# Optimization experiments

Hardware: AMD Instinct MI355X
Metric: run time of the kernel (lower is better)

## Reference

```python
import jax, jax.numpy as jnp
import numpy as np

B = 4; IMG = 32; P = 2; CIN = 3; G = IMG // P; N = G * G; D = 768; NL = 8
DI = 1536; NH = 24; HD = 64; DS = 128; CONVDIM = DI + 2 * DS; DPROJ = 2 * DI + 2 * DS + NH
OUTC = 3 * CIN; FREQ = 256; EPS = 1e-6


def _sincos_1d(dim, pos):
    omega = np.arange(dim // 2, dtype=np.float64) / (dim / 2.0)
    omega = 1.0 / 10000 ** omega
    out = np.einsum('m,d->md', pos.reshape(-1), omega)
    return np.concatenate([np.sin(out), np.cos(out)], axis=1)


def _pos_embed_2d(dim, gs):
    gh = np.arange(gs, dtype=np.float32)
    gw = np.arange(gs, dtype=np.float32)
    grid = np.stack(np.meshgrid(gw, gh), axis=0)
    return np.concatenate([_sincos_1d(dim // 2, grid[0]), _sincos_1d(dim // 2, grid[1])], axis=1)


POS = jnp.asarray(_pos_embed_2d(D, G), dtype=jnp.float32)[None]  # [1, N, D]


def _ln(x):
    m = x.mean(-1, keepdims=True)
    v = ((x - m) ** 2).mean(-1, keepdims=True)
    return (x - m) * jax.lax.rsqrt(v + EPS)


def _patch_embed(img, w, b):
    # conv with kernel=stride=P == reshape to (c, ph, pw)-ordered patch vectors + matmul
    xp = img.reshape(B, CIN, G, P, G, P).transpose(0, 2, 4, 1, 3, 5).reshape(B, N, CIN * P * P)
    return xp @ w + b


def _t_embed(t, tw1, tb1, tw2, tb2):
    half = FREQ // 2
    freqs = jnp.exp(-jnp.log(10000.0) * jnp.arange(half, dtype=jnp.float32) / half)
    args = t[:, None] * freqs[None]
    emb = jnp.concatenate([jnp.cos(args), jnp.sin(args)], axis=-1)
    return jax.nn.silu(emb @ tw1 + tb1) @ tw2 + tb2


def _mamba2(u, in_w, conv_w, conv_b, dt_bias, A_log, D_ssm, out_w):
    # u: [B, N, D]
    zxbcdt = u @ in_w                           # [B, N, DPROJ]
    z = zxbcdt[..., :DI]
    xBC = zxbcdt[..., DI:DI + CONVDIM]
    dt_raw = zxbcdt[..., DI + CONVDIM:]
    # causal depthwise conv1d, kernel 4
    pad = jnp.pad(xBC, ((0, 0), (3, 0), (0, 0)))
    xBC = sum(pad[:, k:k + N, :] * conv_w[:, k] for k in range(4)) + conv_b
    xBC = jax.nn.silu(xBC)
    xs = xBC[..., :DI].reshape(B, N, NH, HD)
    Bm = xBC[..., DI:DI + DS]
    Cm = xBC[..., DI + DS:]
    dt = jax.nn.softplus(dt_raw + dt_bias)       # [B, N, NH]
    a = dt * (-jnp.exp(A_log))                   # [B, N, NH], negative
    acum = jnp.cumsum(a, axis=1)
    seg = acum[:, :, None, :] - acum[:, None, :, :]   # [B, l, s, NH]
    tril = jnp.tril(jnp.ones((N, N), bool))
    decay = jnp.exp(jnp.where(tril[None, :, :, None], seg, -1e30))
    decay = jnp.moveaxis(decay, -1, 1)           # [B, NH, l, s]
    CB = jnp.einsum('bln,bsn->bls', Cm, Bm)
    scores = CB[:, None] * decay * jnp.moveaxis(dt, -1, 1)[:, :, None, :]
    y = jnp.einsum('bhls,bshp->blhp', scores, xs) + D_ssm[None, None, :, None] * xs
    y = y.reshape(B, N, DI) * jax.nn.silu(z)
    return y @ out_w


def _conv3(x, w, b):
    o = jax.lax.conv_general_dilated(x, w, (1, 1), 'SAME',
                                     dimension_numbers=('NCHW', 'OIHW', 'NCHW'))
    return o + b[None, :, None, None]


def _hfnet(h, w1, b1, w2, b2, w3, b3):
    c = jax.nn.relu(_conv3(h, w1, b1))
    c = jax.nn.relu(_conv3(c, w2, b2))
    return h + _conv3(c, w3, b3)


def _forward(x, t, y, H1, H2, H3, xe_w, xe_b, ye_w, ye_b, tw1, tb1, tw2, tb2,
             adaln_w, adaln_b, in_w, conv_w, conv_b, dt_bias, A_log, D_ssm, out_w,
             fl_t_w, fl_t_b, fl_y_w, fl_y_b, fl_lin_w, fl_lin_b,
             e1_w1, e1_b1, e1_w2, e1_b2, e1_w3, e1_b3,
             e2_w1, e2_b1, e2_w2, e2_b2, e2_w3, e2_b3,
             e3_w1, e3_b1, e3_w2, e3_b2, e3_w3, e3_b3):
    xe = _patch_embed(x, xe_w, xe_b) + POS
    ye = _patch_embed(y, ye_w, ye_b) + POS
    te = _t_embed(t, tw1, tb1, tw2, tb2)
    st = jax.nn.silu(te)          # [B, D]
    sy = jax.nn.silu(ye)          # [B, N, D]

    def layer(xc, p):
        aw, ab, iw, cw, cb, db, al, dd, ow = p
        sh_t, sc_t, g_t = jnp.split(st @ aw + ab, 3, axis=-1)
        sh_y, sc_y, g_y = jnp.split(sy @ aw + ab, 3, axis=-1)
        shift = sh_t[:, None] + sh_y
        scale = sc_t[:, None] + sc_y
        gate = g_t[:, None] + g_y
        xm = _ln(xc) * (1.0 + scale) + shift
        return gate * _mamba2(xm, iw, cw, cb, db, al, dd, ow) + xc, None

    xh, _ = jax.lax.scan(layer, xe, (adaln_w, adaln_b, in_w, conv_w, conv_b,
                                     dt_bias, A_log, D_ssm, out_w))
    sh_t, sc_t = jnp.split(st @ fl_t_w + fl_t_b, 2, axis=-1)
    sh_y, sc_y = jnp.split(sy @ fl_y_w + fl_y_b, 2, axis=-1)
    xf = (_ln(xh) * (1.0 + sc_t[:, None] + sc_y) + sh_t[:, None] + sh_y) @ fl_lin_w + fl_lin_b
    # unpatchify: nhwpqc -> nchpwq
    img = xf.reshape(B, G, G, P, P, OUTC).transpose(0, 5, 1, 3, 2, 4).reshape(B, OUTC, IMG, IMG)
    h1 = _hfnet(H1, e1_w1, e1_b1, e1_w2, e1_b2, e1_w3, e1_b3)
    h2 = _hfnet(H2, e2_w1, e2_b1, e2_w2, e2_b2, e2_w3, e2_b3)
    h3 = _hfnet(H3, e3_w1, e3_b1, e3_w2, e3_b2, e3_w3, e3_b3)
    return (img, h1, h2, h3)


def setup_inputs() -> dict:
    ks = iter(jax.random.split(jax.random.key(0), 80))
    def nrm(shape, s=0.02):
        return jax.random.normal(next(ks), shape, jnp.float32) * s
    z = lambda *s: jnp.zeros(s, jnp.float32)
    inp = {}
    inp['x'] = jax.random.normal(next(ks), (B, CIN, IMG, IMG), jnp.float32)
    inp['t'] = jax.random.uniform(next(ks), (B,), jnp.float32) * 1000.0
    inp['y'] = jax.random.normal(next(ks), (B, CIN, IMG, IMG), jnp.float32)
    inp['H1'] = jax.random.normal(next(ks), (B, CIN, IMG, IMG), jnp.float32)
    inp['H2'] = jax.random.normal(next(ks), (B, CIN, IMG, IMG), jnp.float32)
    inp['H3'] = jax.random.normal(next(ks), (B, CIN, IMG, IMG), jnp.float32)
    inp['xe_w'] = nrm((CIN * P * P, D), 0.1); inp['xe_b'] = z(D)
    inp['ye_w'] = nrm((CIN * P * P, D), 0.1); inp['ye_b'] = z(D)
    inp['tw1'] = nrm((FREQ, D)); inp['tb1'] = z(D)
    inp['tw2'] = nrm((D, D)); inp['tb2'] = z(D)
    inp['adaln_w'] = nrm((NL, D, 3 * D)); inp['adaln_b'] = nrm((NL, 3 * D))
    inp['in_w'] = nrm((NL, D, DPROJ))
    inp['conv_w'] = nrm((NL, CONVDIM, 4), 0.2); inp['conv_b'] = z(NL, CONVDIM)
    inp['dt_bias'] = nrm((NL, NH), 0.5)
    inp['A_log'] = jnp.tile(jnp.log(jnp.arange(1.0, NH + 1.0, dtype=jnp.float32)), (NL, 1))
    inp['D_ssm'] = jnp.ones((NL, NH), jnp.float32)
    inp['out_w'] = nrm((NL, DI, D))
    inp['fl_t_w'] = nrm((D, 2 * D)); inp['fl_t_b'] = z(2 * D)
    inp['fl_y_w'] = nrm((D, 2 * D)); inp['fl_y_b'] = z(2 * D)
    inp['fl_lin_w'] = nrm((D, P * P * OUTC)); inp['fl_lin_b'] = z(P * P * OUTC)
    for i in (1, 2, 3):
        inp['e%d_w1' % i] = nrm((64, CIN, 3, 3), 0.1); inp['e%d_b1' % i] = z(64)
        inp['e%d_w2' % i] = nrm((64, 64, 3, 3), 0.05); inp['e%d_b2' % i] = z(64)
        inp['e%d_w3' % i] = nrm((CIN, 64, 3, 3), 0.05); inp['e%d_b3' % i] = z(CIN)
    return inp


def reference(x, t, y, H1, H2, H3, xe_w, xe_b, ye_w, ye_b, tw1, tb1, tw2, tb2,
              adaln_w, adaln_b, in_w, conv_w, conv_b, dt_bias, A_log, D_ssm, out_w,
              fl_t_w, fl_t_b, fl_y_w, fl_y_b, fl_lin_w, fl_lin_b,
              e1_w1, e1_b1, e1_w2, e1_b2, e1_w3, e1_b3,
              e2_w1, e2_b1, e2_w2, e2_b2, e2_w3, e2_b3,
              e3_w1, e3_b1, e3_w2, e3_b2, e3_w3, e3_b3):
    return _forward(x, t, y, H1, H2, H3, xe_w, xe_b, ye_w, ye_b, tw1, tb1, tw2, tb2,
                    adaln_w, adaln_b, in_w, conv_w, conv_b, dt_bias, A_log, D_ssm, out_w,
                    fl_t_w, fl_t_b, fl_y_w, fl_y_b, fl_lin_w, fl_lin_b,
                    e1_w1, e1_b1, e1_w2, e1_b2, e1_w3, e1_b3,
                    e2_w1, e2_b1, e2_w2, e2_b2, e2_w3, e2_b3,
                    e3_w1, e3_b1, e3_w2, e3_b2, e3_w3, e3_b3)
```

## Files before the change

### kernel.cpp

```cpp
#include <hip/hip_runtime.h>
#include <cmath>

namespace {

constexpr int kB = 4;
constexpr int kN = 256;
constexpr int kD = 768;
constexpr int kNL = 8;
constexpr int kDI = 1536;
constexpr int kNH = 24;
constexpr int kHD = 64;
constexpr int kCONV = 1792;
constexpr int kDPROJ = 3352;
constexpr int kD3 = 2304;
constexpr int kNCAT = 19968;
constexpr int kOFF_FL = 18432;

typedef __attribute__((ext_vector_type(8))) short short8;
typedef __attribute__((ext_vector_type(4))) float f32x4;

__device__ __forceinline__ float siluf(float x) { return x / (1.f + expf(-x)); }

__device__ __forceinline__ short f2bf(float f) {
  unsigned u = __float_as_uint(f);
  unsigned r = (u + 0x7fffu + ((u >> 16) & 1u)) >> 16;
  return (short)r;
}

__device__ __forceinline__ void gload_lds16(const void* g, void* l) {
  __builtin_amdgcn_global_load_lds(
      (const __attribute__((address_space(1))) void*)g,
      (__attribute__((address_space(3))) void*)l, 16, 0, 0);
}

template <int N> __device__ __forceinline__ void wait_barrier();
template <> __device__ __forceinline__ void wait_barrier<0>() {
  asm volatile("s_waitcnt vmcnt(0)\n\ts_barrier" ::: "memory");
}
template <> __device__ __forceinline__ void wait_barrier<2>() {
  asm volatile("s_waitcnt vmcnt(2)\n\ts_barrier" ::: "memory");
}
template <> __device__ __forceinline__ void wait_barrier<3>() {
  asm volatile("s_waitcnt vmcnt(3)\n\ts_barrier" ::: "memory");
}
template <> __device__ __forceinline__ void wait_barrier<4>() {
  asm volatile("s_waitcnt vmcnt(4)\n\ts_barrier" ::: "memory");
}

__global__ void patch_embed2_kernel(const float* __restrict__ img0,
                                    const float* __restrict__ w0,
                                    const float* __restrict__ b0,
                                    float* __restrict__ out0,
                                    const float* __restrict__ img1,
                                    const float* __restrict__ w1,
                                    const float* __restrict__ b1,
                                    float* __restrict__ out1,
                                    short* __restrict__ out1_bf) {
  int gid = blockIdx.x * blockDim.x + threadIdx.x;
  if (gid >= kB * kN * kD) return;
  int z = blockIdx.z;
  const float* img = z ? img1 : img0;
  const float* w = z ? w1 : w0;
  const float* bias = z ? b1 : b0;
  int d = gid % kD;
  int n = (gid / kD) % kN;
  int b = gid / (kD * kN);
  int gi = n >> 4, gj = n & 15;
  float acc = bias[d];
#pragma unroll
  for (int c = 0; c < 3; ++c)
#pragma unroll
    for (int pi = 0; pi < 2; ++pi)
#pragma unroll
      for (int pj = 0; pj < 2; ++pj) {
        float v = img[((b * 3 + c) * 32 + gi * 2 + pi) * 32 + gj * 2 + pj];
        acc += v * w[(c * 4 + pi * 2 + pj) * kD + d];
      }
  float pos;
  if (d < 192)       pos = sinf((float)gj * powf(10000.f, -(float)d / 192.f));
  else if (d < 384)  pos = cosf((float)gj * powf(10000.f, -(float)(d - 192) / 192.f));
  else if (d < 576)  pos = sinf((float)gi * powf(10000.f, -(float)(d - 384) / 192.f));
  else               pos = cosf((float)gi * powf(10000.f, -(float)(d - 576) / 192.f));
  acc += pos;
  if (z) {
    float v = siluf(acc);
    out1[gid] = v;
    out1_bf[gid] = f2bf(v);
  } else {
    out0[gid] = acc;
  }
}

__global__ void tembed_args_kernel(const float* __restrict__ t,
                                   float* __restrict__ ctst) {
  int idx = blockIdx.x * 256 + threadIdx.x;
  if (idx >= kB * 256) return;
  int b = idx >> 8, j = idx & 255;
  int k = j & 127;
  float f = expf(-9.210340371976184f * (float)k / 128.f);
  float arg = t[b] * f;
  ctst[idx] = (j < 128) ? cosf(arg) : sinf(arg);
}

__global__ __launch_bounds__(256) void splitk_mm_stage1(
    const float* __restrict__ A, const float* __restrict__ W,
    float* __restrict__ part, int K, int Nn, int KC) {
  int n = blockIdx.x * 256 + threadIdx.x;
  int kc = blockIdx.y;
  int l = blockIdx.z;
  if (n >= Nn) return;
  const float* w = W + (size_t)l * K * Nn + (size_t)kc * 64 * Nn + n;
  int kb = kc * 64;
  float a0 = 0.f, a1 = 0.f, a2 = 0.f, a3 = 0.f;
  for (int k = 0; k < 64; ++k) {
    float wv = w[(size_t)k * Nn];
    a0 += A[0 * K + kb + k] * wv;
    a1 += A[1 * K + kb + k] * wv;
    a2 += A[2 * K + kb + k] * wv;
    a3 += A[3 * K + kb + k] * wv;
  }
  size_t base = (((size_t)l * KC + kc) * 4) * Nn + n;
  part[base] = a0;
  part[base + Nn] = a1;
  part[base + 2 * (size_t)Nn] = a2;
  part[base + 3 * (size_t)Nn] = a3;
}

__global__ void splitk_mm_reduce(const float* __restrict__ part,
                                 const float* __restrict__ bias,
                                 float* __restrict__ C, int Nn, int KC, int L,
                                 int act) {
  int idx = blockIdx.x * 256 + threadIdx.x;
  if (idx >= L * 4 * Nn) return;
  int n = idx % Nn;
  int b = (idx / Nn) & 3;
  int l = idx / (4 * Nn);
  float s = bias[(size_t)l * Nn + n];
  for (int kc = 0; kc < KC; ++kc)
    s += part[(((size_t)l * KC + kc) * 4 + b) * Nn + n];
  C[idx] = act ? siluf(s) : s;
}

__global__ __launch_bounds__(256) void transposeW_kernel(
    const float* __restrict__ W, short* __restrict__ Wt, int K, int N,
    size_t sW, size_t sWt) {
  W += (size_t)blockIdx.z * sW;
  Wt += (size_t)blockIdx.z * sWt;
  __shared__ float tile[32][33];
  int n0 = blockIdx.x * 32, k0 = blockIdx.y * 32;
  int tid = threadIdx.x;
  int tx = tid & 31, ty = tid >> 5;
#pragma unroll
  for (int i = 0; i < 4; ++i) {
    int k = k0 + ty + i * 8;
    int n = n0 + tx;
    tile[ty + i * 8][tx] = (n < N) ? W[(size_t)k * N + n] : 0.f;
  }
  __syncthreads();
#pragma unroll
  for (int i = 0; i < 4; ++i) {
    int n = n0 + ty + i * 8;
    int k = k0 + tx;
    Wt[(size_t)n * K + k] = f2bf(tile[tx][ty + i * 8]);
  }
}

__global__ void concat_bias_kernel(const float* __restrict__ a,
                                   const float* __restrict__ b,
                                   float* __restrict__ dst) {
  int i = blockIdx.x * 256 + threadIdx.x;
  if (i < kOFF_FL) dst[i] = a[i];
  else if (i < kNCAT) dst[i] = b[i - kOFF_FL];
}

template <int BM, int BN>
__global__ __launch_bounds__(256) void mfma_gemm(
    const short* __restrict__ A, const short* __restrict__ Bt,
    const float* __restrict__ bias, float* __restrict__ C,
    int Nn, int Ksplit, int Ktot, int ldc, size_t czstride) {
  constexpr int MI = BM / 32;
  constexpr int NJ = BN / 32;
  constexpr int LPW = BM / 64 + BN / 64;
  __shared__ short Als[3 * BM * 32];
  __shared__ short Bls[3 * BN * 32];
  int m0 = blockIdx.y * BM, n0 = blockIdx.x * BN;
  int koff = blockIdx.z * Ksplit;
  C += (size_t)blockIdx.z * czstride;
  int tid = threadIdx.x;
  int lane = tid & 63, wid = tid >> 6;
  int wr = wid >> 1, wc = wid & 1;
  f32x4 acc[MI][NJ] = {};
  int sm = tid >> 2;
  int sk = (tid & 3) * 8;
  const int nsteps = Ksplit >> 5;
  auto stage = [&](int buf, int k0) {
#pragma unroll
    for (int h = 0; h < BM / 64; ++h)
      gload_lds16(&A[(size_t)(m0 + h * 64 + sm) * Ktot + koff + k0 + sk],
                  &Als[buf * (BM * 32) + h * 2048 + wid * 512]);
#pragma unroll
    for (int h = 0; h < BN / 64; ++h)
      gload_lds16(&Bt[(size_t)(n0 + h * 64 + sm) * Ktot + koff + k0 + sk],
                  &Bls[buf * (BN * 32) + h * 2048 + wid * 512]);
  };
  stage(0, 0);
  if (nsteps > 1) stage(1, 32);
  int cur = 0;
  for (int s = 0; s < nsteps; ++s) {
    if (s + 1 < nsteps) wait_barrier<LPW>();
    else wait_barrier<0>();
    if (s + 2 < nsteps) stage(cur == 0 ? 2 : cur - 1, (s + 2) << 5);
    short8 av[MI], bv[NJ];
#pragma unroll
    for (int mi = 0; mi < MI; ++mi)
      av[mi] = *(const short8*)&Als[cur * (BM * 32) +
                                    (wr * (BM / 2) + mi * 16 + (lane & 15)) *
                                        32 +
                                    (lane >> 4) * 8];
#pragma unroll
    for (int nj = 0; nj < NJ; ++nj)
      bv[nj] = *(const short8*)&Bls[cur * (BN * 32) +
                                    (wc * (BN / 2) + nj * 16 + (lane & 15)) *
                                        32 +
                                    (lane >> 4) * 8];
#pragma unroll
    for (int mi = 0; mi < MI; ++mi)
#pragma unroll
      for (int nj = 0; nj < NJ; ++nj)
        acc[mi][nj] = __builtin_amdgcn_mfma_f32_16x16x32_bf16(
            av[mi], bv[nj], acc[mi][nj], 0, 0, 0);
    cur = (cur == 2) ? 0 : cur + 1;
  }
#pragma unroll
  for (int mi = 0; mi < MI; ++mi)
#pragma unroll
    for (int nj = 0; nj < NJ; ++nj)
#pragma unroll
      for (int r = 0; r < 4; ++r) {
        int gm = m0 + wr * (BM / 2) + mi * 16 + (lane >> 4) * 4 + r;
        int gn = n0 + wc * (BN / 2) + nj * 16 + (lane & 15);
        if (gn >= Nn) continue;
        C[(size_t)gm * ldc + gn] = acc[mi][nj][r] + (bias ? bias[gn] : 0.f);
      }
}

__global__ __launch_bounds__(256) void cb_mfma_kernel(
    const short* __restrict__ bC, const short* __restrict__ bB,
    float* __restrict__ CBp) {
  constexpr int K = 128;
  __shared__ short Als[128 * 32];
  __shared__ short Bls[128 * 32];
  int b = blockIdx.z;
  int m0 = blockIdx.y * 128, n0 = blockIdx.x * 128;
  if (n0 >= m0 + 128) return;
  const short* A = bC + (size_t)b * 256 * K;
  const short* Bt = bB + (size_t)b * 256 * K;
  int tid = threadIdx.x;
  int lane = tid & 63, wid = tid >> 6;
  int wr = wid >> 1, wc = wid & 1;
  f32x4 acc[4][4] = {};
  int sm = tid >> 2;
  int sk = (tid & 3) * 8;
  for (int k0 = 0; k0 < K; k0 += 32) {
    __syncthreads();
    gload_lds16(&A[(size_t)(m0 + sm) * K + k0 + sk], &Als[wid * 512]);
    gload_lds16(&A[(size_t)(m0 + 64 + sm) * K + k0 + sk],
                &Als[2048 + wid * 512]);
    gload_lds16(&Bt[(size_t)(n0 + sm) * K + k0 + sk], &Bls[wid * 512]);
    gload_lds16(&Bt[(size_t)(n0 + 64 + sm) * K + k0 + sk],
                &Bls[2048 + wid * 512]);
    __syncthreads();
    short8 av[4], bv[4];
#pragma unroll
    for (int mi = 0; mi < 4; ++mi)
      av[mi] = *(const short8*)&Als[(wr * 64 + mi * 16 + (lane & 15)) * 32 +
                                    (lane >> 4) * 8];
#pragma unroll
    for (int nj = 0; nj < 4; ++nj)
      bv[nj] = *(const short8*)&Bls[(wc * 64 + nj * 16 + (lane & 15)) * 32 +
                                    (lane >> 4) * 8];
#pragma unroll
    for (int mi = 0; mi < 4; ++mi)
#pragma unroll
      for (int nj = 0; nj < 4; ++nj)
        acc[mi][nj] = __builtin_amdgcn_mfma_f32_16x16x32_bf16(
            av[mi], bv[nj], acc[mi][nj], 0, 0, 0);
  }
#pragma unroll
  for (int mi = 0; mi < 4; ++mi)
#pragma unroll
    for (int nj = 0; nj < 4; ++nj)
#pragma unroll
      for (int r = 0; r < 4; ++r) {
        int gm = m0 + wr * 64 + mi * 16 + (lane >> 4) * 4 + r;
        int gn = n0 + wc * 64 + nj * 16 + (lane & 15);
        CBp[((size_t)(b * 256 + gm)) * 256 + gn] = acc[mi][nj][r];
      }
}

__global__ __launch_bounds__(256) void ln_mod_kernel(
    const float* __restrict__ x, const float* __restrict__ tA,
    const float* __restrict__ yA, short* __restrict__ out_bf, int tstride,
    int ystride, const float* __restrict__ p0, const float* __restrict__ p1,
    const float* __restrict__ gtA, const float* __restrict__ gyA,
    float* __restrict__ xcw) {
  int row = blockIdx.x;
  int b = row >> 8;
  __shared__ float xr[kD];
  __shared__ float red[256];
  int tid = threadIdx.x;
  float s = 0.f;
  for (int i = tid; i < kD; i += 256) {
    float v = x[(size_t)row * kD + i];
    if (p0) {
      float g = gtA[b * kD3 + 2 * kD + i] +
                gyA[(size_t)row * kNCAT + 2 * kD + i];
      v += g * (p0[(size_t)row * kD + i] + p1[(size_t)row * kD + i]);
      xcw[(size_t)row * kD + i] = v;
    }
    xr[i] = v;
    s += v;
  }
  red[tid] = s;
  __syncthreads();
  for (int o = 128; o > 0; o >>= 1) {
    if (tid < o) red[tid] += red[tid + o];
    __syncthreads();
  }
  float mean = red[0] / (float)kD;
  __syncthreads();
  float s2 = 0.f;
  for (int i = tid; i < kD; i += 256) {
    float d = xr[i] - mean;
    s2 += d * d;
  }
  red[tid] = s2;
  __syncthreads();
  for (int o = 128; o > 0; o >>= 1) {
    if (tid < o) red[tid] += red[tid + o];
    __syncthreads();
  }
  float rstd = rsqrtf(red[0] / (float)kD + 1e-6f);
  for (int i = tid; i < kD; i += 256) {
    float sc = tA[b * tstride + kD + i] + yA[(size_t)row * ystride + kD + i];
    float sh = tA[b * tstride + i] + yA[(size_t)row * ystride + i];
    float v = (xr[i] - mean) * rstd * (1.f + sc) + sh;
    out_bf[(size_t)row * kD + i] = f2bf(v);
  }
}

__global__ __launch_bounds__(256) void convdt_kernel(
    const float* __restrict__ zx, const float* __restrict__ cw,
    const float* __restrict__ cb, const float* __restrict__ db,
    const float* __restrict__ al, float* __restrict__ xbc,
    short* __restrict__ bB, short* __restrict__ bC, float* __restrict__ dts,
    float* __restrict__ acum) {
  constexpr int kConvBlocks = kB * kN * kCONV / 256;
  int blk = blockIdx.x;
  if (blk < kConvBlocks) {
    int idx = blk * 256 + threadIdx.x;
    int c = idx % kCONV;
    int row = idx / kCONV;
    int n = row & 255, b = row >> 8;
    float acc = cb[c];
#pragma unroll
    for (int k = 0; k < 4; ++k) {
      int ns = n + k - 3;
      if (ns >= 0)
        acc += zx[(size_t)(b * kN + ns) * kDPROJ + kDI + c] * cw[c * 4 + k];
    }
    float v = siluf(acc);
    xbc[idx] = v;
    if (c >= kDI) {
      if (c < kDI + 128)
        bB[(size_t)row * 128 + (c - kDI)] = f2bf(v);
      else
        bC[(size_t)row * 128 + (c - kDI - 128)] = f2bf(v);
    }
  } else {
    int bh = blk - kConvBlocks;
    int b = bh / kNH, h = bh % kNH;
    int n = threadIdx.x;
    __shared__ float sb[256];
    size_t row = (size_t)(b * kN + n);
    float xv = zx[row * kDPROJ + (kDI + kCONV) + h] + db[h];
    float dt = xv > 20.f ? xv : log1pf(expf(xv));
    dts[row * kNH + h] = dt;
    float a = -expf(al[h]) * dt;
    sb[n] = a;
    __syncthreads();
    for (int off = 1; off < 256; off <<= 1) {
      float v = (n >= off) ? sb[n - off] : 0.f;
      __syncthreads();
      sb[n] += v;
      __syncthreads();
    }
    acum[row * kNH + h] = sb[n];
  }
}

__global__ __launch_bounds__(256) void ssm_y_kernel(
    const float* __restrict__ CBp, const float* __restrict__ acum,
    const float* __restrict__ dts, const float* __restrict__ xbc,
    const float* __restrict__ zx, const float* __restrict__ Dssm,
    short* __restrict__ ybuf) {
  int bh = blockIdx.z;
  int b = bh / kNH, h = bh % kNH;
  int m0 = blockIdx.y * 64;
  int tid = threadIdx.x;
  int tx = tid & 15, ty = tid >> 4;
  __shared__ float As[16][65];
  __shared__ float Xs[16][64];
  float acc[4][4] = {};
  for (int k0 = 0; k0 < kN; k0 += 16) {
    if (k0 > m0 + 63) break;
#pragma unroll
    for (int i = 0; i < 4; ++i) {
      int e = tid + i * 256;
      int m = e >> 4, k = e & 15;
      int l = m0 + m, ss = k0 + k;
      float v = 0.f;
      if (ss <= l) {
        float dec = expf(acum[(size_t)(b * kN + l) * kNH + h] -
                         acum[(size_t)(b * kN + ss) * kNH + h]);
        v = CBp[(size_t)(b * kN + l) * kN + ss] * dec *
            dts[(size_t)(b * kN + ss) * kNH + h];
      }
      As[k][m] = v;
    }
#pragma unroll
    for (int i = 0; i < 4; ++i) {
      int e = tid + i * 256;
      int k = e >> 6, n = e & 63;
      Xs[k][n] = xbc[(size_t)(b * kN + k0 + k) * kCONV + h * kHD + n];
    }
    __syncthreads();
#pragma unroll
    for (int kk = 0; kk < 16; ++kk) {
      float a[4], bb[4];
#pragma unroll
      for (int i = 0; i < 4; ++i) a[i] = As[kk][ty * 4 + i];
#pragma unroll
      for (int j = 0; j < 4; ++j) bb[j] = Xs[kk][tx * 4 + j];
#pragma unroll
      for (int i = 0; i < 4; ++i)
#pragma unroll
        for (int j = 0; j < 4; ++j) acc[i][j] += a[i] * bb[j];
    }
    __syncthreads();
  }
  float dd = Dssm[h];
#pragma unroll
  for (int i = 0; i < 4; ++i) {
    int l = m0 + ty * 4 + i;
    size_t row = (size_t)(b * kN + l);
#pragma unroll
    for (int j = 0; j < 4; ++j) {
      int p = tx * 4 + j;
      int col = h * kHD + p;
      float xs_l = xbc[row * kCONV + col];
      float yv = acc[i][j] + dd * xs_l;
      float zv = zx[row * kDPROJ + col];
      ybuf[row * kDI + col] = f2bf(yv * siluf(zv));
    }
  }
}

__global__ void unpatchify_kernel(const float* __restrict__ fpp,
                                  const float* __restrict__ bias,
                                  float* __restrict__ out) {
  constexpr int kFP = kB * kN * 36;
  int gid = blockIdx.x * 256 + threadIdx.x;
  if (gid >= kFP) return;
  int j = gid % 36;
  int row = gid / 36;
  int n = row & 255, b = row >> 8;
  int o = j % 9;
  int pj = (j / 9) & 1;
  int pi = j / 18;
  int gi = n >> 4, gj = n & 15;
  float v = fpp[gid] + fpp[kFP + gid] + fpp[2 * kFP + gid] +
            fpp[3 * kFP + gid] + bias[j];
  out[((b * 9 + o) * 32 + gi * 2 + pi) * 32 + (gj * 2 + pj)] = v;
}

__global__ __launch_bounds__(256) void conv1_kernel(
    const float* __restrict__ Ha, const float* __restrict__ Hb,
    const float* __restrict__ Hc, const float* __restrict__ wa,
    const float* __restrict__ wb, const float* __restrict__ wc,
    const float* __restrict__ ba, const float* __restrict__ bb,
    const float* __restrict__ bc, short* __restrict__ dst) {
  int gid = blockIdx.x * 256 + threadIdx.x;
  if (gid >= 3 * 4096 * 64) return;
  int oc = gid & 63;
  int px = (gid >> 6) & 4095;
  int net = gid >> 18;
  const float* in = net == 0 ? Ha : (net == 1 ? Hb : Hc);
  const float* w = net == 0 ? wa : (net == 1 ? wb : wc);
  const float* bs = net == 0 ? ba : (net == 1 ? bb : bc);
  int xx = px & 31, yy = (px >> 5) & 31, b = px >> 10;
  float acc = bs[oc];
#pragma unroll
  for (int ic = 0; ic < 3; ++ic) {
    const float* ip = in + ((size_t)(b * 3 + ic) << 10);
    const float* wp = w + (oc * 3 + ic) * 9;
#pragma unroll
    for (int ky = 0; ky < 3; ++ky) {
      int ys = yy + ky - 1;
      if (ys < 0 || ys > 31) continue;
#pragma unroll
      for (int kx = 0; kx < 3; ++kx) {
        int xs = xx + kx - 1;
        if (xs < 0 || xs > 31) continue;
        acc += ip[ys * 32 + xs] * wp[ky * 3 + kx];
      }
    }
  }
  dst[gid] = f2bf(fmaxf(acc, 0.f));
}

__global__ __launch_bounds__(256) void convw_prep_kernel(
    const float* __restrict__ w2a, const float* __restrict__ w2b,
    const float* __restrict__ w2c, const float* __restrict__ w3a,
    const float* __restrict__ w3b, const float* __restrict__ w3c,
    short* __restrict__ dst2, short* __restrict__ dst3) {
  int idx = blockIdx.x * 256 + threadIdx.x;
  if (idx >= 3 * 128 * 576) return;
  int z = blockIdx.z;
  int OC = z ? 3 : 64;
  short* dst = z ? dst3 : dst2;
  int k = idx % 576;
  int row = (idx / 576) & 127;
  int net = idx / (128 * 576);
  const float* w = z ? (net == 0 ? w3a : (net == 1 ? w3b : w3c))
                     : (net == 0 ? w2a : (net == 1 ? w2b : w2c));
  int pos = k >> 6, ic = k & 63;
  float v = (row < OC) ? w[row * 576 + ic * 9 + pos] : 0.f;
  dst[idx] = f2bf(v);
}

template <int EP>
__global__ __launch_bounds__(256) void conv_gemm(
    const short* __restrict__ src, const short* __restrict__ Btall,
    const float* __restrict__ b_a, const float* __restrict__ b_b,
    const float* __restrict__ b_c, const float* __restrict__ r_a,
    const float* __restrict__ r_b, const float* __restrict__ r_c,
    short* __restrict__ dst, float* __restrict__ outp) {
  constexpr int K = 576;
  __shared__ short Als[128 * 32];
  __shared__ short Bls[128 * 32];
  int net = blockIdx.z;
  int m0 = blockIdx.y * 128;
  const float* bias = net == 0 ? b_a : (net == 1 ? b_b : b_c);
  const float* res = net == 0 ? r_a : (net == 1 ? r_b : r_c);
  const short* Bt = Btall + (size_t)net * 128 * K;
  int tid = threadIdx.x;
  int lane = tid & 63, wid = tid >> 6;
  int wr = wid >> 1, wc = wid & 1;
  f32x4 acc[4][4] = {};
  int sm = tid >> 2;
  int sk = (tid & 3) * 8;
  for (int k0 = 0; k0 < K; k0 += 32) {
    int kk = k0 + sk;
    int pos = kk >> 6, ic0 = kk & 63;
    int ky = pos / 3 - 1, kx = pos % 3 - 1;
    uint4 a_st[2], b_st[2];
#pragma unroll
    for (int i = 0; i < 2; ++i) {
      int px = m0 + i * 64 + sm;
      int b = px >> 10;
      int yy = (px >> 5) & 31, xx = px & 31;
      int ys = yy + ky, xs = xx + kx;
      if (ys >= 0 && ys < 32 && xs >= 0 && xs < 32) {
        a_st[i] = *(const uint4*)&src[((size_t)(net * 4096 + (b << 10) +
                                                (ys << 5) + xs)
                                       << 6) +
                                      ic0];
      } else {
        a_st[i] = make_uint4(0u, 0u, 0u, 0u);
      }
      b_st[i] = *(const uint4*)&Bt[(size_t)(i * 64 + sm) * K + kk];
    }
    __syncthreads();
    *(uint4*)&Als[sm * 32 + sk] = a_st[0];
    *(uint4*)&Als[(64 + sm) * 32 + sk] = a_st[1];
    *(uint4*)&Bls[sm * 32 + sk] = b_st[0];
    *(uint4*)&Bls[(64 + sm) * 32 + sk] = b_st[1];
    __syncthreads();
    short8 av[4], bv[4];
#pragma unroll
    for (int mi = 0; mi < 4; ++mi)
      av[mi] = *(const short8*)&Als[(wr * 64 + mi * 16 + (lane & 15)) * 32 +
                                    (lane >> 4) * 8];
#pragma unroll
    for (int nj = 0; nj < 4; ++nj)
      bv[nj] = *(const short8*)&Bls[(wc * 64 + nj * 16 + (lane & 15)) * 32 +
                                    (lane >> 4) * 8];
#pragma unroll
    for (int mi = 0; mi < 4; ++mi)
#pragma unroll
      for (int nj = 0; nj < 4; ++nj)
        acc[mi][nj] = __builtin_amdgcn_mfma_f32_16x16x32_bf16(
            av[mi], bv[nj], acc[mi][nj], 0, 0, 0);
  }
#pragma unroll
  for (int mi = 0; mi < 4; ++mi)
#pragma unroll
    for (int nj = 0; nj < 4; ++nj)
#pragma unroll
      for (int r = 0; r < 4; ++r) {
        int gm = m0 + wr * 64 + mi * 16 + (lane >> 4) * 4 + r;
        int gn = wc * 64 + nj * 16 + (lane & 15);
        float v = acc[mi][nj][r];
        if (EP == 0) {
          if (gn < 64)
            dst[(size_t)(net * 4096 + gm) * 64 + gn] =
                f2bf(fmaxf(v + bias[gn], 0.f));
        } else {
          if (gn < 3) {
            int b = gm >> 10, pix = gm & 1023;
            size_t o = (size_t)(b * 3 + gn) * 1024 + pix;
            outp[36864 + net * 12288 + o] = v + bias[gn] + res[o];
          }
        }
      }
}

}

extern "C" void kernel_launch(void* const* d_in, const int* in_sizes, int n_in,
                              void* d_out, int out_size, void* d_ws,
                              size_t ws_size, hipStream_t stream) {
  const float* x = (const float*)d_in[0];
  const float* t = (const float*)d_in[1];
  const float* y = (const float*)d_in[2];
  const float* H[3] = {(const float*)d_in[3], (const float*)d_in[4],
                       (const float*)d_in[5]};
  const float* xe_w = (const float*)d_in[6];
  const float* xe_b = (const float*)d_in[7];
  const float* ye_w = (const float*)d_in[8];
  const float* ye_b = (const float*)d_in[9];
  const float* tw1 = (const float*)d_in[10];
  const float* tb1 = (const float*)d_in[11];
  const float* tw2 = (const float*)d_in[12];
  const float* tb2 = (const float*)d_in[13];
  const float* adaln_w = (const float*)d_in[14];
  const float* adaln_b = (const float*)d_in[15];
  const float* in_w = (const float*)d_in[16];
  const float* conv_w = (const float*)d_in[17];
  const float* conv_b = (const float*)d_in[18];
  const float* dt_bias = (const float*)d_in[19];
  const float* A_log = (const float*)d_in[20];
  const float* D_ssm = (const float*)d_in[21];
  const float* out_w = (const float*)d_in[22];
  const float* fl_t_w = (const float*)d_in[23];
  const float* fl_t_b = (const float*)d_in[24];
  const float* fl_y_w = (const float*)d_in[25];
  const float* fl_y_b = (const float*)d_in[26];
  const float* fl_lin_w = (const float*)d_in[27];
  const float* fl_lin_b = (const float*)d_in[28];

  float* out = (float*)d_out;
  float* ws = (float*)d_ws;

  size_t off = 0;
  auto alloc = [&](size_t nelem) { float* p = ws + off; off += nelem; return p; };
  float* xc    = alloc((size_t)kB * kN * kD);
  float* sy    = alloc((size_t)kB * kN * kD);
  short* sy_bf = (short*)alloc((size_t)kB * kN * kD / 2);
  float* st    = alloc((size_t)kB * kD);
  float* ht    = alloc((size_t)kB * kD);
  float* ctst  = alloc((size_t)kB * 256);
  float* tAall = alloc((size_t)kNL * kB * kD3);
  float* yA8   = alloc((size_t)kB * kN * kNCAT);
  short* xm_bf = (short*)alloc((size_t)kB * kN * kD / 2);
  float* zx    = alloc((size_t)kB * kN * kDPROJ);
  float* xbc   = alloc((size_t)kB * kN * kCONV);
  float* dts   = alloc((size_t)kB * kN * kNH);
  float* acum  = alloc((size_t)kB * kN * kNH);
  float* CBp   = alloc((size_t)kB * kN * kN);
  short* ybuf  = (short*)alloc((size_t)kB * kN * kDI / 2);
  float* tfl   = alloc((size_t)kB * 2 * kD);
  float* opart = alloc((size_t)2 * kB * kN * kD);
  float* fpp   = alloc((size_t)4 * kB * kN * 36);
  short* adalnT = (short*)alloc((size_t)kNCAT * kD / 2);
  float* biascat = alloc(kNCAT);
  short* in_wT = (short*)alloc((size_t)kNL * 3456 * kD / 2);
  short* Wt    = (short*)alloc((size_t)128 * kD / 2);
  short* bBm   = (short*)alloc((size_t)kB * kN * 128 / 2);
  short* bCm   = (short*)alloc((size_t)kB * kN * 128 / 2);
  short* c1bf  = (short*)alloc((size_t)3 * 4096 * 64 / 2);
  short* c2bf  = (short*)alloc((size_t)3 * 4096 * 64 / 2);
  short* Bt2   = (short*)alloc((size_t)3 * 128 * 576 / 2);
  short* Bt3   = (short*)alloc((size_t)3 * 128 * 576 / 2);
  (void)ws_size;

  float* part = zx;
  short* out_wT = adalnT;

  dim3 blk(256);

  patch_embed2_kernel<<<dim3((kB * kN * kD + 255) / 256, 1, 2), blk, 0,
                        stream>>>(x, xe_w, xe_b, xc, y, ye_w, ye_b, sy, sy_bf);

  transposeW_kernel<<<dim3(72, 24, kNL), blk, 0, stream>>>(
      adaln_w, adalnT, kD, kD3, (size_t)kD * kD3, (size_t)kD3 * kD);
  transposeW_kernel<<<dim3(48, 24, 1), blk, 0, stream>>>(
      fl_y_w, adalnT + (size_t)kOFF_FL * kD, kD, 2 * kD, 0, 0);
  concat_bias_kernel<<<dim3((kNCAT + 255) / 256), blk, 0, stream>>>(
      adaln_b, fl_y_b, biascat);
  mfma_gemm<128, 128><<<dim3(kNCAT / 128, 8), blk, 0, stream>>>(
      sy_bf, adalnT, biascat, yA8, kNCAT, kD, kD, kNCAT, 0);

  transposeW_kernel<<<dim3(108, 24, kNL), blk, 0, stream>>>(
      in_w, in_wT, kD, kDPROJ, (size_t)kD * kDPROJ, (size_t)3456 * kD);
  transposeW_kernel<<<dim3(24, 48, kNL), blk, 0, stream>>>(
      out_w, out_wT, kDI, kD, (size_t)kDI * kD, (size_t)768 * kDI);

  tembed_args_kernel<<<dim3(4), blk, 0, stream>>>(t, ctst);
  splitk_mm_stage1<<<dim3(3, 4, 1), blk, 0, stream>>>(ctst, tw1, part, 256,
                                                      kD, 4);
  splitk_mm_reduce<<<dim3((kB * kD + 255) / 256), blk, 0, stream>>>(
      part, tb1, ht, kD, 4, 1, 1);
  splitk_mm_stage1<<<dim3(3, 12, 1), blk, 0, stream>>>(ht, tw2, part, kD, kD, 12);
  splitk_mm_reduce<<<dim3((kB * kD + 255) / 256), blk, 0, stream>>>(
      part, tb2, st, kD, 12, 1, 1);
  splitk_mm_stage1<<<dim3(9, 12, kNL), blk, 0, stream>>>(st, adaln_w, part, kD,
                                                         kD3, 12);
  splitk_mm_reduce<<<dim3((kNL * kB * kD3 + 255) / 256), blk, 0, stream>>>(
      part, adaln_b, tAall, kD3, 12, kNL, 0);
  splitk_mm_stage1<<<dim3(6, 12, 1), blk, 0, stream>>>(st, fl_t_w, part, kD,
                                                       2 * kD, 12);
  splitk_mm_reduce<<<dim3((kB * 2 * kD + 255) / 256), blk, 0, stream>>>(
      part, fl_t_b, tfl, 2 * kD, 12, 1, 0);

  for (int l = 0; l < kNL; ++l) {
    const float* cw = conv_w + (size_t)l * kCONV * 4;
    const float* cb = conv_b + (size_t)l * kCONV;
    const float* db = dt_bias + (size_t)l * kNH;
    const float* al = A_log + (size_t)l * kNH;
    const float* dd = D_ssm + (size_t)l * kNH;
    float* tA = tAall + (size_t)l * kB * kD3;
    const float* yAl = yA8 + (size_t)l * kD3;
    const float* ptA = l ? tAall + (size_t)(l - 1) * kB * kD3 : nullptr;
    const float* pyA = l ? yA8 + (size_t)(l - 1) * kD3 : nullptr;

    ln_mod_kernel<<<dim3(kB * kN), blk, 0, stream>>>(
        xc, tA, yAl, xm_bf, kD3, kNCAT, l ? opart : nullptr,
        l ? opart + (size_t)kB * kN * kD : nullptr, ptA, pyA, xc);
    mfma_gemm<64, 64><<<dim3(54, 16), blk, 0, stream>>>(
        xm_bf, in_wT + (size_t)l * 3456 * kD, nullptr, zx, kDPROJ, kD, kD,
        kDPROJ, 0);
    convdt_kernel<<<dim3(kB * kN * kCONV / 256 + kB * kNH), blk, 0, stream>>>(
        zx, cw, cb, db, al, xbc, bBm, bCm, dts, acum);
    cb_mfma_kernel<<<dim3(2, 2, kB), blk, 0, stream>>>(bCm, bBm, CBp);
    ssm_y_kernel<<<dim3(1, kN / 64, kB * kNH), blk, 0, stream>>>(
        CBp, acum, dts, xbc, zx, dd, ybuf);
    mfma_gemm<64, 64><<<dim3(12, 16, 2), blk, 0, stream>>>(
        ybuf, out_wT + (size_t)l * 768 * kDI, nullptr, opart, kD, kD, kDI,
        kD, (size_t)kB * kN * kD);
  }

  ln_mod_kernel<<<dim3(kB * kN), blk, 0, stream>>>(
      xc, tfl, yA8 + kOFF_FL, xm_bf, 2 * kD, kNCAT, opart,
      opart + (size_t)kB * kN * kD, tAall + (size_t)7 * kB * kD3,
      yA8 + (size_t)7 * kD3, xc);
  transposeW_kernel<<<dim3(4, 24, 1), blk, 0, stream>>>(fl_lin_w, Wt, kD, 36,
                                                        0, 0);
  mfma_gemm<64, 128><<<dim3(1, 16, 4), blk, 0, stream>>>(
      xm_bf, Wt, nullptr, fpp, 36, 192, kD, 36, (size_t)kB * kN * 36);
  unpatchify_kernel<<<dim3((kB * kN * 36 + 255) / 256), blk, 0, stream>>>(
      fpp, fl_lin_b, out);

  const float* w1s[3] = {(const float*)d_in[29], (const float*)d_in[35],
                         (const float*)d_in[41]};
  const float* b1s[3] = {(const float*)d_in[30], (const float*)d_in[36],
                         (const float*)d_in[42]};
  const float* w2s[3] = {(const float*)d_in[31], (const float*)d_in[37],
                         (const float*)d_in[43]};
  const float* b2s[3] = {(const float*)d_in[32], (const float*)d_in[38],
                         (const float*)d_in[44]};
  const float* w3s[3] = {(const float*)d_in[33], (const float*)d_in[39],
                         (const float*)d_in[45]};
  const float* b3s[3] = {(const float*)d_in[34], (const float*)d_in[40],
                         (const float*)d_in[46]};
  convw_prep_kernel<<<dim3((3 * 128 * 576 + 255) / 256, 1, 2), blk, 0,
                      stream>>>(w2s[0], w2s[1], w2s[2], w3s[0], w3s[1],
                                w3s[2], Bt2, Bt3);
  conv1_kernel<<<dim3(3 * 4096 * 64 / 256), blk, 0, stream>>>(
      H[0], H[1], H[2], w1s[0], w1s[1], w1s[2], b1s[0], b1s[1], b1s[2], c1bf);
  conv_gemm<0><<<dim3(1, 32, 3), blk, 0, stream>>>(
      c1bf, Bt2, b2s[0], b2s[1], b2s[2], nullptr, nullptr, nullptr, c2bf,
      nullptr);
  conv_gemm<1><<<dim3(1, 32, 3), blk, 0, stream>>>(
      c2bf, Bt3, b3s[0], b3s[1], b3s[2], H[0], H[1], H[2], nullptr, out);
}
```

Baseline: 1.146 ms.

## Deepen GEMM LDS pipeline to four stages and remap blocks across XCDs

The bf16 MFMA GEMM now keeps three k-tiles in flight using a four-buffer LDS ring instead of three, with matching vmcnt waits. This gives more memory latency hiding per block. It also remaps linear block IDs so that consecutive tiles land on the same XCD chunk, which should improve L2 reuse across the 8 XCDs. The cost is more LDS per block, which may lower occupancy, and the remap only applies when the block count is a multiple of 8.

```diff
diff --git a/kernel.cpp b/kernel.cpp
--- a/kernel.cpp
+++ b/kernel.cpp
@@ -45,6 +45,12 @@
 }
 template <> __device__ __forceinline__ void wait_barrier<4>() {
   asm volatile("s_waitcnt vmcnt(4)\n\ts_barrier" ::: "memory");
+}
+template <> __device__ __forceinline__ void wait_barrier<6>() {
+  asm volatile("s_waitcnt vmcnt(6)\n\ts_barrier" ::: "memory");
+}
+template <> __device__ __forceinline__ void wait_barrier<8>() {
+  asm volatile("s_waitcnt vmcnt(8)\n\ts_barrier" ::: "memory");
 }
 
 __global__ void patch_embed2_kernel(const float* __restrict__ img0,
@@ -181,9 +187,22 @@
   constexpr int MI = BM / 32;
   constexpr int NJ = BN / 32;
   constexpr int LPW = BM / 64 + BN / 64;
-  __shared__ short Als[3 * BM * 32];
-  __shared__ short Bls[3 * BN * 32];
-  int m0 = blockIdx.y * BM, n0 = blockIdx.x * BN;
+  __shared__ short Als[4 * BM * 32];
+  __shared__ short Bls[4 * BN * 32];
+  int gx = gridDim.x, gy = gridDim.y;
+  int nblk = gx * gy;
+  int hl = blockIdx.y * gx + blockIdx.x;
+  int txi, tyi;
+  if ((nblk & 7) == 0) {
+    int chunk = nblk >> 3;
+    int s_id = (hl & 7) * chunk + (hl >> 3);
+    txi = s_id / gy;
+    tyi = s_id % gy;
+  } else {
+    txi = blockIdx.x;
+    tyi = blockIdx.y;
+  }
+  int m0 = tyi * BM, n0 = txi * BN;
   int koff = blockIdx.z * Ksplit;
   C += (size_t)blockIdx.z * czstride;
   int tid = threadIdx.x;
@@ -205,11 +224,13 @@
   };
   stage(0, 0);
   if (nsteps > 1) stage(1, 32);
-  int cur = 0;
+  if (nsteps > 2) stage(2, 64);
   for (int s = 0; s < nsteps; ++s) {
-    if (s + 1 < nsteps) wait_barrier<LPW>();
+    int cur = s & 3;
+    if (s + 2 < nsteps) wait_barrier<2 * LPW>();
+    else if (s + 1 < nsteps) wait_barrier<LPW>();
     else wait_barrier<0>();
-    if (s + 2 < nsteps) stage(cur == 0 ? 2 : cur - 1, (s + 2) << 5);
+    if (s + 3 < nsteps) stage((s + 3) & 3, (s + 3) << 5);
     short8 av[MI], bv[NJ];
 #pragma unroll
     for (int mi = 0; mi < MI; ++mi)
@@ -229,7 +250,6 @@
       for (int nj = 0; nj < NJ; ++nj)
         acc[mi][nj] = __builtin_amdgcn_mfma_f32_16x16x32_bf16(
             av[mi], bv[nj], acc[mi][nj], 0, 0, 0);
-    cur = (cur == 2) ? 0 : cur + 1;
   }
 #pragma unroll
   for (int mi = 0; mi < MI; ++mi)
```

New measurement: 1.162 ms. No clear change (+1.4%).
